# Kernel optimization log

Measured on AMD Instinct MI355X. Metric: run time of the kernel, lower is better.

Reference implementation:

```python
import jax, jax.numpy as jnp
import numpy as np

B, Q, L = 64, 64, 8192
KC = 51            # NarrowConv1D kernel size
HC = KC // 2 + 1   # 26 raw symmetric-half params
N = 500
KT = N + 1         # 501 transpose-conv kernel size
HT = KT // 2 + 1   # 251 raw half params

@jax.custom_vjp
def sigmoid_st(u):
    # Sigmoid forward, straight-through (identity) backward
    return jax.nn.sigmoid(u)

def _sst_fwd(u):
    return jax.nn.sigmoid(u), None

def _sst_bwd(res, g):
    return (g,)

sigmoid_st.defvjp(_sst_fwd, _sst_bwd)

def symmetric(w):
    # cat(X, X[..., :-1].flip(-1)) -> symmetric kernel of odd length
    return jnp.concatenate([w, w[..., :-1][..., ::-1]], axis=-1)

def depthwise_conv(x, k, pad):
    # x: [B, Q, L]; k: [Q, K] one kernel per channel (groups == channels)
    return jax.lax.conv_general_dilated(
        x, k[:, None, :], window_strides=(1,), padding=[(pad, pad)],
        dimension_numbers=("NCH", "OIH", "NCH"), feature_group_count=x.shape[1])

def setup_inputs() -> dict:
    key = jax.random.key(0)
    k1, k2, k3, k4 = jax.random.split(key, 4)
    return {
        "x": jax.random.normal(k1, (B, Q, L), dtype=jnp.float32),
        "conv_w_half": jax.random.normal(k2, (HC,), dtype=jnp.float32) * 0.1,
        "tc_w_half": jax.random.normal(k3, (Q, HT), dtype=jnp.float32),
        "A_raw": jax.random.normal(k4, (Q,), dtype=jnp.float32),
    }

def reference(x, conv_w_half, tc_w_half, A_raw):
    # 1) NarrowConv1D: one symmetric kernel shared across all Q channels
    kc = symmetric(conv_w_half)                       # [51]
    kc_full = jnp.broadcast_to(kc, (Q, KC))           # ChannelSame expand
    x = depthwise_conv(x, kc_full, KC // 2)           # [B,Q,L], 'same'

    # 2) softmax over spectral axis
    x = jax.nn.softmax(x, axis=-1)

    # 3) SymmetricNormConvTranspose1d: sigmoid(straight-through) + symmetric;
    #    stride-1 transpose conv with symmetric kernel == depthwise conv with
    #    padding K-1-p = N//2
    wt = sigmoid_st(tc_w_half)                        # [Q, 251] in (0,1)
    kt = symmetric(wt)                                # [Q, 501]
    x = depthwise_conv(x, kt, N // 2)                 # [B,Q,L]

    # 4) serial lattice (reflection/transmission) recursion over Q channels
    a = sigmoid_st(A_raw)                             # [Q]
    xs = jnp.transpose(x, (1, 0, 2))                  # [Q,B,L]

    def step(carry, inp):
        r, t2 = carry
        rn, aq = inp
        tn = 1.0 - rn
        s = 1.0 / (1.0 - aq * r * rn)
        r_new = r + aq * rn * t2 * s
        t2_new = aq * t2 * tn * tn * s * s
        return (r_new, t2_new), None

    init = (jnp.zeros_like(xs[0]), jnp.ones_like(xs[0]))
    (r, _), _ = jax.lax.scan(step, init, (xs, a))

    peak = wt[-1, -1]                                 # weight[-1,0,N//2] (kernel center)
    r = r / (peak * jnp.prod(a))
    return r                                          # [B, L]
```

## Files before the change

### kernel.cpp

```cpp
#include <hip/hip_runtime.h>

#define B_ 64
#define Q_ 64
#define L_ 8192
#define KCONV 51
#define HC 26
#define HT 251
#define NCH2 34
#define NCH1 6
#define TAL_CH 28

#define A51_OFF 512
#define TA_OFF  8192
#define RN_OFF  2236416

#define MAPB(s) ((((s) & ~7) | ((((s) & 7) + ((s) >> 3)) & 7)) << 4)

typedef _Float16 f16x8 __attribute__((ext_vector_type(8)));
typedef float f32x16 __attribute__((ext_vector_type(16)));
typedef const __attribute__((address_space(1))) void cg_void;
typedef __attribute__((address_space(3))) void lds_void3;

__device__ __forceinline__ float sigm(float v) {
    return 1.0f / (1.0f + __expf(-v));
}

__global__ __launch_bounds__(256) void k_params(const float* __restrict__ cwh,
                                                const float* __restrict__ tcw,
                                                const float* __restrict__ araw,
                                                float* __restrict__ ws) {
    const int tid = threadIdx.x;
    const int q = blockIdx.x;
    char* wsb = (char*)ws;
    if (q < Q_) {
        for (int idx = tid; idx < NCH2 * 64; idx += 256) {
            int c = idx >> 6, lane = idx & 63;
            int hi = lane >> 5, i = lane & 31;
            int mbase = 16 * c + 8 * hi - i - 6;
            f16x8 hv;
            #pragma unroll
            for (int jj = 0; jj < 8; jj++) {
                int m = mbase + jj;
                float v = 0.0f;
                if (m >= 0 && m <= 500) {
                    int hh = (m <= 250) ? m : (500 - m);
                    v = sigm(tcw[q * HT + hh]);
                }
                hv[jj] = (_Float16)v;
            }
            *(f16x8*)(wsb + TA_OFF + ((size_t)q * (NCH2 * 64) + idx) * 16) = hv;
        }
    } else {
        if (tid < Q_) ws[tid] = sigm(araw[tid]);
        for (int idx = tid; idx < NCH1 * 64; idx += 256) {
            int c = idx >> 6, lane = idx & 63;
            int hi = lane >> 5, i = lane & 31;
            int mbase = 16 * c + 8 * hi - i - 7;
            f16x8 hv;
            #pragma unroll
            for (int jj = 0; jj < 8; jj++) {
                int m = mbase + jj;
                float v = 0.0f;
                if (m >= 0 && m < KCONV) v = cwh[m < HC ? m : (KCONV - 1 - m)];
                hv[jj] = (_Float16)v;
            }
            *(f16x8*)(wsb + A51_OFF + idx * 16) = hv;
        }
        __syncthreads();
        if (tid == 0) {
            float p = 1.0f;
            for (int j = 0; j < Q_; j++) p *= ws[j];
            float peak = sigm(tcw[(Q_ - 1) * HT + 250]);
            ws[64] = 1.0f / (peak * p);
        }
    }
}

__global__ __launch_bounds__(512, 4) void k_fused(const float* __restrict__ x,
                                                  float* __restrict__ ws) {
    const int tid = threadIdx.x;
    const int bid = blockIdx.x;
    const int q = bid >> 5, pr = bid & 31;
    const int row0 = (2 * pr) * Q_ + q, row1 = (2 * pr + 1) * Q_ + q;
    char* wsb = (char*)ws;
    __shared__ __attribute__((aligned(128))) char bufA[17408];
    __shared__ __attribute__((aligned(128))) char bufB[17408];
    __shared__ __attribute__((aligned(128))) char TAL[TAL_CH * 1024];
    __shared__ float red[32];

    const int w = tid >> 6, lane = tid & 63, j = lane & 31, hi = lane >> 5;

    {
        const char* tabg = wsb + TA_OFF + (size_t)q * (NCH2 * 64) * 16;
        for (int c = w; c < TAL_CH; c += 8) {
            const void* gp = tabg + (c * 64 + lane) * 16;
            __builtin_amdgcn_global_load_lds((cg_void*)gp,
                                             (lds_void3*)(TAL + c * 1024), 16, 0, 0);
        }
    }

    const uint4 z4 = {0u, 0u, 0u, 0u};
    if (tid < 32) {
        *(uint4*)(bufA + MAPB(tid)) = z4;
        *(uint4*)(bufB + MAPB(tid)) = z4;
    } else if (tid >= 64 && tid < 96) {
        int s = 1056 + (tid - 64);
        *(uint4*)(bufA + MAPB(s)) = z4;
        *(uint4*)(bufB + MAPB(s)) = z4;
    }

    union H8 { _Float16 h[8]; uint4 u; };
    {
        const float* xr0 = x + (size_t)row0 * L_ + 16 * tid;
        const float* xr1 = x + (size_t)row1 * L_ + 16 * tid;
        #pragma unroll
        for (int r = 0; r < 2; r++) {
            const float* xr = r ? xr1 : xr0;
            char* buf = r ? bufB : bufA;
            float4 f0 = *(const float4*)(xr + 0);
            float4 f1 = *(const float4*)(xr + 4);
            float4 f2 = *(const float4*)(xr + 8);
            float4 f3 = *(const float4*)(xr + 12);
            H8 h0, h1;
            h0.h[0] = (_Float16)f0.x; h0.h[1] = (_Float16)f0.y;
            h0.h[2] = (_Float16)f0.z; h0.h[3] = (_Float16)f0.w;
            h0.h[4] = (_Float16)f1.x; h0.h[5] = (_Float16)f1.y;
            h0.h[6] = (_Float16)f1.z; h0.h[7] = (_Float16)f1.w;
            h1.h[0] = (_Float16)f2.x; h1.h[1] = (_Float16)f2.y;
            h1.h[2] = (_Float16)f2.z; h1.h[3] = (_Float16)f2.w;
            h1.h[4] = (_Float16)f3.x; h1.h[5] = (_Float16)f3.y;
            h1.h[6] = (_Float16)f3.z; h1.h[7] = (_Float16)f3.w;
            *(uint4*)(buf + MAPB(2 * tid + 32)) = h0.u;
            *(uint4*)(buf + MAPB(2 * tid + 33)) = h1.u;
        }
    }
    __syncthreads();

    f32x16 acc0 = {}, acc1 = {};
    {
        #pragma unroll
        for (int c = 0; c < NCH1; c++) {
            f16x8 a51 = *(const f16x8*)(wsb + A51_OFF + (c * 64 + lane) * 16);
            const int bo = MAPB(128 * w + 4 * j + 2 * c + 28 + hi);
            f16x8 bf0 = *(const f16x8*)(bufA + bo);
            f16x8 bf1 = *(const f16x8*)(bufB + bo);
            acc0 = __builtin_amdgcn_mfma_f32_32x32x16_f16(a51, bf0, acc0, 0, 0, 0);
            acc1 = __builtin_amdgcn_mfma_f32_32x32x16_f16(a51, bf1, acc1, 0, 0, 0);
        }
    }

    float mx0 = -3.402823466e+38f, mx1 = -3.402823466e+38f;
    #pragma unroll
    for (int e = 0; e < 16; e++) { mx0 = fmaxf(mx0, acc0[e]); mx1 = fmaxf(mx1, acc1[e]); }
    #pragma unroll
    for (int o = 32; o > 0; o >>= 1) {
        mx0 = fmaxf(mx0, __shfl_xor(mx0, o));
        mx1 = fmaxf(mx1, __shfl_xor(mx1, o));
    }
    if (lane == 0) { red[w] = mx0; red[8 + w] = mx1; }
    __syncthreads();
    mx0 = red[0]; mx1 = red[8];
    #pragma unroll
    for (int i = 1; i < 8; i++) { mx0 = fmaxf(mx0, red[i]); mx1 = fmaxf(mx1, red[8 + i]); }
    float sm0 = 0.0f, sm1 = 0.0f;
    #pragma unroll
    for (int e = 0; e < 16; e++) {
        acc0[e] = __expf(acc0[e] - mx0); sm0 += acc0[e];
        acc1[e] = __expf(acc1[e] - mx1); sm1 += acc1[e];
    }
    #pragma unroll
    for (int o = 32; o > 0; o >>= 1) { sm0 += __shfl_xor(sm0, o); sm1 += __shfl_xor(sm1, o); }
    if (lane == 0) { red[16 + w] = sm0; red[24 + w] = sm1; }
    __syncthreads();
    float s0 = red[16], s1 = red[24];
    #pragma unroll
    for (int i = 1; i < 8; i++) { s0 += red[16 + i]; s1 += red[24 + i]; }
    const float isum0 = 1.0f / s0, isum1 = 1.0f / s1;

    union P4 { _Float16 h[4]; uint2 u; };
    #pragma unroll
    for (int k = 0; k < 4; k++) {
        P4 p0, p1;
        #pragma unroll
        for (int d = 0; d < 4; d++) {
            p0.h[d] = (_Float16)(acc0[4 * k + d] * isum0);
            p1.h[d] = (_Float16)(acc1[4 * k + d] * isum1);
        }
        const int bo = MAPB(128 * w + 4 * j + k + 32) + 8 * hi;
        *(uint2*)(bufA + bo) = p0.u;
        *(uint2*)(bufB + bo) = p1.u;
    }
    __syncthreads();

    const char* tab6 = wsb + TA_OFF + ((size_t)q * (NCH2 * 64) + lane) * 16;
    f32x16 o0 = {}, o1 = {};
    #pragma unroll
    for (int c = 0; c < NCH2; c++) {
        f16x8 af = (c < TAL_CH)
            ? *(const f16x8*)(TAL + c * 1024 + lane * 16)
            : *(const f16x8*)(tab6 + c * 1024);
        const int bo = MAPB(128 * w + 4 * j + 2 * c + hi);
        f16x8 bf0 = *(const f16x8*)(bufA + bo);
        f16x8 bf1 = *(const f16x8*)(bufB + bo);
        o0 = __builtin_amdgcn_mfma_f32_32x32x16_f16(af, bf0, o0, 0, 0, 0);
        o1 = __builtin_amdgcn_mfma_f32_32x32x16_f16(af, bf1, o1, 0, 0, 0);
    }
    __syncthreads();

    #pragma unroll
    for (int k = 0; k < 4; k++) {
        P4 p0, p1;
        #pragma unroll
        for (int d = 0; d < 4; d++) {
            p0.h[d] = (_Float16)o0[4 * k + d];
            p1.h[d] = (_Float16)o1[4 * k + d];
        }
        const int bo = MAPB(128 * w + 4 * j + k) + 8 * hi;
        *(uint2*)(bufA + bo) = p0.u;
        *(uint2*)(bufB + bo) = p1.u;
    }
    __syncthreads();
    {
        uint4 r0 = *(uint4*)(bufA + MAPB(2 * tid));
        uint4 r1 = *(uint4*)(bufA + MAPB(2 * tid + 1));
        char* dst = wsb + RN_OFF + ((size_t)row0 * L_ + 16 * tid) * 2;
        *(uint4*)dst = r0;
        *(uint4*)(dst + 16) = r1;
        uint4 r2 = *(uint4*)(bufB + MAPB(2 * tid));
        uint4 r3 = *(uint4*)(bufB + MAPB(2 * tid + 1));
        char* dst1 = wsb + RN_OFF + ((size_t)row1 * L_ + 16 * tid) * 2;
        *(uint4*)dst1 = r2;
        *(uint4*)(dst1 + 16) = r3;
    }
}

__global__ __launch_bounds__(256) void k_lat(const float* __restrict__ ws,
                                             float* __restrict__ out) {
    const int tid = threadIdx.x;
    const int T = blockIdx.x & 7, b = blockIdx.x >> 3;
    const char* wsb = (const char*)ws;
    const int l = 1024 * T + 4 * tid;
    const char* src = wsb + RN_OFF + ((size_t)(b * Q_) * L_ + l) * 2;
    float r[4] = {0.0f, 0.0f, 0.0f, 0.0f};
    float t2[4] = {1.0f, 1.0f, 1.0f, 1.0f};
    union P4 { _Float16 h[4]; uint2 u; };
    P4 cur;
    cur.u = *(const uint2*)src;
    for (int q = 0; q < Q_; q++) {
        P4 nxt = cur;
        if (q < Q_ - 1) nxt.u = *(const uint2*)(src + (size_t)(q + 1) * L_ * 2);
        const float aq = ws[q];
        #pragma unroll
        for (int e = 0; e < 4; e++) {
            float rn = (float)cur.h[e], tn = 1.0f - rn;
            float si = 1.0f / (1.0f - aq * r[e] * rn);
            float rnew = r[e] + aq * rn * t2[e] * si;
            t2[e] = aq * t2[e] * tn * tn * si * si;
            r[e] = rnew;
        }
        cur = nxt;
    }
    const float inv_scale = ws[64];
    float4 o;
    o.x = r[0] * inv_scale; o.y = r[1] * inv_scale;
    o.z = r[2] * inv_scale; o.w = r[3] * inv_scale;
    *(float4*)&out[(size_t)b * L_ + l] = o;
}

extern "C" void kernel_launch(void* const* d_in, const int* in_sizes, int n_in,
                              void* d_out, int out_size, void* d_ws, size_t ws_size,
                              hipStream_t stream) {
    (void)in_sizes; (void)n_in; (void)out_size; (void)ws_size;
    const float* x    = (const float*)d_in[0];
    const float* cwh  = (const float*)d_in[1];
    const float* tcw  = (const float*)d_in[2];
    const float* araw = (const float*)d_in[3];
    float* out = (float*)d_out;
    float* ws  = (float*)d_ws;

    hipLaunchKernelGGL(k_params, dim3(Q_ + 1), dim3(256), 0, stream, cwh, tcw, araw, ws);
    hipLaunchKernelGGL(k_fused, dim3((B_ / 2) * Q_), dim3(512), 0, stream, x, ws);
    hipLaunchKernelGGL(k_lat, dim3(B_ * 8), dim3(256), 0, stream, ws, out);
}
```

Measured before the change: 97.85 us.

## Software-pipeline MFMA operand loads and merge softmax max/sum reductions

Hoists the conv51 weight loads before the LDS staging and software-pipelines the B-operand and A-table loads in both MFMA loops with register double/quad buffering, so LDS and global latency overlaps with MFMA issue. Also fuses the cross-wave max and sum reductions of the softmax into a single barrier using the online-softmax rescaling trick, removing one __syncthreads. Adds register pressure and a few extra exps per thread, which could lower occupancy.

```diff
diff --git a/kernel.cpp b/kernel.cpp
--- a/kernel.cpp
+++ b/kernel.cpp
@@ -99,6 +99,11 @@
         }
     }
 
+    f16x8 a51r[NCH1];
+    #pragma unroll
+    for (int c = 0; c < NCH1; c++)
+        a51r[c] = *(const f16x8*)(wsb + A51_OFF + (c * 64 + lane) * 16);
+
     const uint4 z4 = {0u, 0u, 0u, 0u};
     if (tid < 32) {
         *(uint4*)(bufA + MAPB(tid)) = z4;
@@ -111,11 +116,9 @@
 
     union H8 { _Float16 h[8]; uint4 u; };
     {
-        const float* xr0 = x + (size_t)row0 * L_ + 16 * tid;
-        const float* xr1 = x + (size_t)row1 * L_ + 16 * tid;
         #pragma unroll
         for (int r = 0; r < 2; r++) {
-            const float* xr = r ? xr1 : xr0;
+            const float* xr = x + (size_t)(r ? row1 : row0) * L_ + 16 * tid;
             char* buf = r ? bufB : bufA;
             float4 f0 = *(const float4*)(xr + 0);
             float4 f1 = *(const float4*)(xr + 4);
@@ -138,14 +141,20 @@
 
     f32x16 acc0 = {}, acc1 = {};
     {
+        f16x8 pA[2], pB[2];
+        pA[0] = *(const f16x8*)(bufA + MAPB(128 * w + 4 * j + 28 + hi));
+        pB[0] = *(const f16x8*)(bufB + MAPB(128 * w + 4 * j + 28 + hi));
+        pA[1] = *(const f16x8*)(bufA + MAPB(128 * w + 4 * j + 30 + hi));
+        pB[1] = *(const f16x8*)(bufB + MAPB(128 * w + 4 * j + 30 + hi));
         #pragma unroll
         for (int c = 0; c < NCH1; c++) {
-            f16x8 a51 = *(const f16x8*)(wsb + A51_OFF + (c * 64 + lane) * 16);
-            const int bo = MAPB(128 * w + 4 * j + 2 * c + 28 + hi);
-            f16x8 bf0 = *(const f16x8*)(bufA + bo);
-            f16x8 bf1 = *(const f16x8*)(bufB + bo);
-            acc0 = __builtin_amdgcn_mfma_f32_32x32x16_f16(a51, bf0, acc0, 0, 0, 0);
-            acc1 = __builtin_amdgcn_mfma_f32_32x32x16_f16(a51, bf1, acc1, 0, 0, 0);
+            acc0 = __builtin_amdgcn_mfma_f32_32x32x16_f16(a51r[c], pA[c & 1], acc0, 0, 0, 0);
+            acc1 = __builtin_amdgcn_mfma_f32_32x32x16_f16(a51r[c], pB[c & 1], acc1, 0, 0, 0);
+            if (c + 2 < NCH1) {
+                const int bo = MAPB(128 * w + 4 * j + 2 * (c + 2) + 28 + hi);
+                pA[c & 1] = *(const f16x8*)(bufA + bo);
+                pB[c & 1] = *(const f16x8*)(bufB + bo);
+            }
         }
     }
 
@@ -157,11 +166,6 @@
         mx0 = fmaxf(mx0, __shfl_xor(mx0, o));
         mx1 = fmaxf(mx1, __shfl_xor(mx1, o));
     }
-    if (lane == 0) { red[w] = mx0; red[8 + w] = mx1; }
-    __syncthreads();
-    mx0 = red[0]; mx1 = red[8];
-    #pragma unroll
-    for (int i = 1; i < 8; i++) { mx0 = fmaxf(mx0, red[i]); mx1 = fmaxf(mx1, red[8 + i]); }
     float sm0 = 0.0f, sm1 = 0.0f;
     #pragma unroll
     for (int e = 0; e < 16; e++) {
@@ -170,12 +174,22 @@
     }
     #pragma unroll
     for (int o = 32; o > 0; o >>= 1) { sm0 += __shfl_xor(sm0, o); sm1 += __shfl_xor(sm1, o); }
-    if (lane == 0) { red[16 + w] = sm0; red[24 + w] = sm1; }
-    __syncthreads();
-    float s0 = red[16], s1 = red[24];
-    #pragma unroll
-    for (int i = 1; i < 8; i++) { s0 += red[16 + i]; s1 += red[24 + i]; }
-    const float isum0 = 1.0f / s0, isum1 = 1.0f / s1;
+    if (lane == 0) {
+        red[w] = mx0; red[8 + w] = sm0;
+        red[16 + w] = mx1; red[24 + w] = sm1;
+    }
+    __syncthreads();
+    float mg0 = red[0], mg1 = red[16];
+    #pragma unroll
+    for (int i = 1; i < 8; i++) { mg0 = fmaxf(mg0, red[i]); mg1 = fmaxf(mg1, red[16 + i]); }
+    float ss0 = 0.0f, ss1 = 0.0f;
+    #pragma unroll
+    for (int i = 0; i < 8; i++) {
+        ss0 += red[8 + i] * __expf(red[i] - mg0);
+        ss1 += red[24 + i] * __expf(red[16 + i] - mg1);
+    }
+    const float isum0 = __expf(mx0 - mg0) / ss0;
+    const float isum1 = __expf(mx1 - mg1) / ss1;
 
     union P4 { _Float16 h[4]; uint2 u; };
     #pragma unroll
@@ -194,16 +208,32 @@
 
     const char* tab6 = wsb + TA_OFF + ((size_t)q * (NCH2 * 64) + lane) * 16;
     f32x16 o0 = {}, o1 = {};
-    #pragma unroll
-    for (int c = 0; c < NCH2; c++) {
-        f16x8 af = (c < TAL_CH)
-            ? *(const f16x8*)(TAL + c * 1024 + lane * 16)
-            : *(const f16x8*)(tab6 + c * 1024);
-        const int bo = MAPB(128 * w + 4 * j + 2 * c + hi);
-        f16x8 bf0 = *(const f16x8*)(bufA + bo);
-        f16x8 bf1 = *(const f16x8*)(bufB + bo);
-        o0 = __builtin_amdgcn_mfma_f32_32x32x16_f16(af, bf0, o0, 0, 0, 0);
-        o1 = __builtin_amdgcn_mfma_f32_32x32x16_f16(af, bf1, o1, 0, 0, 0);
+    {
+        f16x8 afr[4], pA[2], pB[2];
+        #pragma unroll
+        for (int c = 0; c < 4; c++)
+            afr[c] = *(const f16x8*)(TAL + c * 1024 + lane * 16);
+        #pragma unroll
+        for (int c = 0; c < 2; c++) {
+            const int bo = MAPB(128 * w + 4 * j + 2 * c + hi);
+            pA[c] = *(const f16x8*)(bufA + bo);
+            pB[c] = *(const f16x8*)(bufB + bo);
+        }
+        #pragma unroll
+        for (int c = 0; c < NCH2; c++) {
+            o0 = __builtin_amdgcn_mfma_f32_32x32x16_f16(afr[c & 3], pA[c & 1], o0, 0, 0, 0);
+            o1 = __builtin_amdgcn_mfma_f32_32x32x16_f16(afr[c & 3], pB[c & 1], o1, 0, 0, 0);
+            if (c + 2 < NCH2) {
+                const int bo = MAPB(128 * w + 4 * j + 2 * (c + 2) + hi);
+                pA[c & 1] = *(const f16x8*)(bufA + bo);
+                pB[c & 1] = *(const f16x8*)(bufB + bo);
+            }
+            if (c + 4 < NCH2) {
+                afr[c & 3] = (c + 4 < TAL_CH)
+                    ? *(const f16x8*)(TAL + (c + 4) * 1024 + lane * 16)
+                    : *(const f16x8*)(tab6 + (c + 4) * 1024);
+            }
+        }
     }
     __syncthreads();
 
```

After: 95.37 us. 1.03x faster.
